# Kernel optimization log

Hardware: AMD Instinct MI355X
Metric: run time of the kernel (lower is better)

## Reference

```python
import jax, jax.numpy as jnp
import numpy as np


def setup_inputs() -> dict:
    key = jax.random.key(0)
    kq, kk, kv, km = jax.random.split(key, 4)
    B, H, S, D = 2, 16, 2048, 64
    Q = jax.random.normal(kq, (B, H, S, D), dtype=jnp.float32)
    K = jax.random.normal(kk, (B, H, S, D), dtype=jnp.float32)
    V = jax.random.normal(kv, (B, H, S, D), dtype=jnp.float32)
    mask = jax.random.randint(km, (B, 1, S, S), 0, 2).astype(jnp.bool_)
    return {"Q": Q, "K": K, "V": V, "mask": mask}


def reference(Q, K, V, mask):
    # scores: [B, H, Sq, Sk]
    scores = jnp.einsum("bhqd,bhkd->bhqk", Q, K)
    neg = jnp.finfo(scores.dtype).min
    # Faithful to original: mask fill happens BEFORE the sqrt(d) scaling.
    scores = jnp.where(mask, neg, scores)
    inv_sqrt_d = 1.0 / jnp.sqrt(jnp.asarray(Q.shape[-1], dtype=scores.dtype))
    attn = jax.nn.softmax(scores * inv_sqrt_d, axis=-1)
    return jnp.einsum("bhqk,bhkd->bhqd", attn, V)
```

## Files before the change

### kernel.cpp

```cpp
#include <hip/hip_runtime.h>
#include <stdint.h>


#define SQ 2048
#define DH 64

using bf16x8  = __attribute__((ext_vector_type(8)))  __bf16;
using f32x4   = __attribute__((ext_vector_type(4)))  float;
using ushort8 = __attribute__((ext_vector_type(8)))  unsigned short;
using ushort4v= __attribute__((ext_vector_type(4)))  unsigned short;
using u32x4   = __attribute__((ext_vector_type(4)))  unsigned int;

static __device__ __forceinline__ unsigned short f2bf(float f) {
    union { float f; uint32_t u; } c; c.f = f;
    return (unsigned short)((c.u + 0x8000u) >> 16);
}

static __device__ __forceinline__ uint32_t pkbf(float a, float b) {
    union { __bf16 h[2]; uint32_t u; } t;
    t.h[0] = (__bf16)a; t.h[1] = (__bf16)b;
    return t.u;
}

static __device__ __forceinline__ f32x4 mfma16(bf16x8 a, bf16x8 b, f32x4 c) {
    return __builtin_amdgcn_mfma_f32_16x16x32_bf16(a, b, c, 0, 0, 0);
}

static __device__ __forceinline__ void gload16(const void* g, void* l) {
    __builtin_amdgcn_global_load_lds(
        (const __attribute__((address_space(1))) void*)g,
        (__attribute__((address_space(3))) void*)l, 16, 0, 0);
}

__global__ __launch_bounds__(256)
void prep_kernel(const int* __restrict__ mask, const float* __restrict__ K,
                 const float* __restrict__ V, unsigned long long* __restrict__ words,
                 unsigned short* __restrict__ Kb, unsigned short* __restrict__ Vt) {
    __shared__ unsigned short tl[64][66];
    const int bx  = blockIdx.x;
    const int tid = threadIdx.x;
    if (bx < 32768) {
        int gid = bx * 256 + tid;
        int mv = mask[gid];
        unsigned long long b = __ballot(mv != 0);
        if ((gid & 63) == 0) words[gid >> 6] = b;
    } else if (bx < 36864) {
        int gid = (bx - 32768) * 256 + tid;
        float4 v = ((const float4*)K)[gid];
        ushort4v t;
        t[0]=f2bf(v.x); t[1]=f2bf(v.y); t[2]=f2bf(v.z); t[3]=f2bf(v.w);
        ((ushort4v*)Kb)[gid] = t;
    } else {
        const int vbx = bx - 36864;
        const int kt  = vbx & 31;
        const size_t bh = vbx >> 5;
        const float* vp = V + (bh * SQ + (size_t)kt * 64) * DH;
        #pragma unroll
        for (int i = 0; i < 4; ++i) {
            int idx = tid + 256 * i;
            int key = idx >> 4;
            int dc  = (idx & 15) * 4;
            float4 v = *(const float4*)(vp + (size_t)key * DH + dc);
            tl[key][dc + 0] = f2bf(v.x);
            tl[key][dc + 1] = f2bf(v.y);
            tl[key][dc + 2] = f2bf(v.z);
            tl[key][dc + 3] = f2bf(v.w);
        }
        __syncthreads();
        unsigned short* op = Vt + bh * DH * SQ + (size_t)kt * 64;
        #pragma unroll
        for (int i = 0; i < 4; ++i) {
            int idx = tid + 256 * i;
            int d  = idx >> 4;
            int m  = idx & 15;
            int kc = m * 4;
            int pos = 32 * (m >> 3) + 8 * (m & 3) + 4 * ((m >> 2) & 1);
            ushort4v t;
            t[0] = tl[kc + 0][d]; t[1] = tl[kc + 1][d];
            t[2] = tl[kc + 2][d]; t[3] = tl[kc + 3][d];
            *(ushort4v*)(op + (size_t)d * SQ + pos) = t;
        }
    }
}

__global__ __launch_bounds__(256, 4)
void attn_kernel(const float* __restrict__ Q,
                 const unsigned short* __restrict__ Kb,
                 const unsigned short* __restrict__ Vtg,
                 const unsigned long long* __restrict__ Mw,
                 float* __restrict__ out) {
    __shared__ __align__(16) unsigned short Ks[2][64 * 64];
    __shared__ __align__(16) unsigned short Vs[2][64 * 64];

    const int tid  = threadIdx.x;
    const int w    = tid >> 6;
    const int l    = tid & 63;
    const int quad = l >> 4;
    const int c16  = l & 15;
    const int bx = blockIdx.x;
    const int hh = bx & 15;
    const int b  = (bx >> 4) & 1;
    const int qt = bx >> 5;

    const size_t bh = (size_t)b * 16 + hh;
    const float* Qp = Q + bh * SQ * DH;
    const int qw = qt * 64 + 16 * w;

    const unsigned long long* Mrow = Mw + ((size_t)b * SQ + qw + c16) * (SQ / 64);

    const int s0 = (2 * w) * 64 + l;
    const int s1 = (2 * w + 1) * 64 + l;
    const int r0 = s0 >> 3, g0s = s0 & 7;
    const int r1 = s1 >> 3, g1s = s1 & 7;
    const char* Kg = (const char*)(Kb  + bh * (size_t)SQ * DH);
    const char* Vg = (const char*)(Vtg + bh * (size_t)DH * SQ);
    const char* kSrc0 = Kg + r0 * 128  + ((g0s ^ (r0 & 7)) << 4);
    const char* kSrc1 = Kg + r1 * 128  + ((g1s ^ (r1 & 7)) << 4);
    const char* vSrc0 = Vg + r0 * 4096 + ((g0s ^ (r0 & 7)) << 4);
    const char* vSrc1 = Vg + r1 * 4096 + ((g1s ^ (r1 & 7)) << 4);

    bf16x8 qf[2];
    {
        const float* qr = Qp + (size_t)(qw + c16) * DH;
        #pragma unroll
        for (int c = 0; c < 2; ++c) {
            int d0 = 32 * c + 8 * quad;
            float4 a  = *(const float4*)(qr + d0);
            float4 b4 = *(const float4*)(qr + d0 + 4);
            ushort8 t;
            t[0]=f2bf(a.x);  t[1]=f2bf(a.y);  t[2]=f2bf(a.z);  t[3]=f2bf(a.w);
            t[4]=f2bf(b4.x); t[5]=f2bf(b4.y); t[6]=f2bf(b4.z); t[7]=f2bf(b4.w);
            qf[c] = __builtin_bit_cast(bf16x8, t);
        }
    }

    f32x4 o[4];
    float lsum = 0.f;
    #pragma unroll
    for (int i = 0; i < 4; ++i) o[i] = (f32x4)(0.f);

    const int xg = (c16 & 7);
    int gfrag[2];
    #pragma unroll
    for (int c = 0; c < 2; ++c) gfrag[c] = ((4 * c + quad) ^ xg) << 3;

    unsigned long long mw = Mrow[0];
    gload16(kSrc0, &Ks[0][(2 * w) * 512]);
    gload16(kSrc1, &Ks[0][(2 * w + 1) * 512]);
    gload16(vSrc0, &Vs[0][(2 * w) * 512]);
    gload16(vSrc1, &Vs[0][(2 * w + 1) * 512]);
    kSrc0 += 8192; kSrc1 += 8192; vSrc0 += 128; vSrc1 += 128;
    __syncthreads();

    for (int t = 0; t < 32; ++t) {
        const int cur = t & 1;

        unsigned long long nmw = 0;
        if (t < 31) {
            gload16(kSrc0, &Ks[cur ^ 1][(2 * w) * 512]);
            gload16(kSrc1, &Ks[cur ^ 1][(2 * w + 1) * 512]);
            gload16(vSrc0, &Vs[cur ^ 1][(2 * w) * 512]);
            gload16(vSrc1, &Vs[cur ^ 1][(2 * w + 1) * 512]);
            kSrc0 += 8192; kSrc1 += 8192; vSrc0 += 128; vSrc1 += 128;
            nmw = Mrow[t + 1];
        }

        const unsigned short* Kc = Ks[cur];
        const unsigned short* Vc = Vs[cur];

        f32x4 s[4];
        #pragma unroll
        for (int i = 0; i < 4; ++i) s[i] = (f32x4)(0.f);
        __builtin_amdgcn_s_setprio(1);
        #pragma unroll
        for (int c = 0; c < 2; ++c) {
            #pragma unroll
            for (int nb = 0; nb < 4; ++nb) {
                bf16x8 kb = __builtin_bit_cast(bf16x8,
                    *(const ushort8*)&Kc[(c16 + 16 * nb) * 64 + gfrag[c]]);
                s[nb] = mfma16(kb, qf[c], s[nb]);
            }
        }
        __builtin_amdgcn_s_setprio(0);

        uint32_t pk[4][2];
        {
            const unsigned long long sh = mw >> (4 * quad);
            #pragma unroll
            for (int nb = 0; nb < 4; ++nb) {
                float pv[4];
                #pragma unroll
                for (int r = 0; r < 4; ++r) {
                    float e = __builtin_amdgcn_exp2f(fmaf(s[nb][r], 0.18033688f, -5.7707802f));
                    pv[r] = ((sh >> (16 * nb + r)) & 1ull) ? 0.0f : e;
                    lsum += pv[r];
                }
                pk[nb][0] = pkbf(pv[0], pv[1]);
                pk[nb][1] = pkbf(pv[2], pv[3]);
            }
        }

        bf16x8 pa[2];
        #pragma unroll
        for (int c = 0; c < 2; ++c) {
            u32x4 tv;
            tv[0] = pk[2 * c][0];     tv[1] = pk[2 * c][1];
            tv[2] = pk[2 * c + 1][0]; tv[3] = pk[2 * c + 1][1];
            pa[c] = __builtin_bit_cast(bf16x8, tv);
        }

        __builtin_amdgcn_s_setprio(1);
        #pragma unroll
        for (int c = 0; c < 2; ++c) {
            #pragma unroll
            for (int db = 0; db < 4; ++db) {
                bf16x8 vb = __builtin_bit_cast(bf16x8,
                    *(const ushort8*)&Vc[(c16 + 16 * db) * 64 + gfrag[c]]);
                o[db] = mfma16(vb, pa[c], o[db]);
            }
        }
        __builtin_amdgcn_s_setprio(0);

        __syncthreads();
        mw = nmw;
    }

    float v = lsum;
    v += __shfl_xor(v, 16, 64);
    v += __shfl_xor(v, 32, 64);
    const float rinv = 1.0f / v;
    float* op = out + (bh * SQ + (size_t)(qw + c16)) * DH + 4 * quad;
    #pragma unroll
    for (int db = 0; db < 4; ++db) {
        float4 st;
        st.x = o[db][0] * rinv; st.y = o[db][1] * rinv;
        st.z = o[db][2] * rinv; st.w = o[db][3] * rinv;
        *(float4*)(op + 16 * db) = st;
    }
}

extern "C" void kernel_launch(void* const* d_in, const int* in_sizes, int n_in,
                              void* d_out, int out_size, void* d_ws, size_t ws_size,
                              hipStream_t stream) {
    const float* Q    = (const float*)d_in[0];
    const float* K    = (const float*)d_in[1];
    const float* V    = (const float*)d_in[2];
    const int*   mask = (const int*)d_in[3];
    float* out = (float*)d_out;

    char* ws = (char*)d_ws;
    unsigned long long* mwords = (unsigned long long*)ws;
    unsigned short* Kb = (unsigned short*)(ws + (1 << 20));
    unsigned short* Vt = (unsigned short*)(ws + (1 << 20) + (8 << 20));

    prep_kernel<<<dim3(37888), dim3(256), 0, stream>>>(mask, K, V, mwords, Kb, Vt);
    attn_kernel<<<dim3(1024), dim3(256), 0, stream>>>(Q, Kb, Vt, mwords, out);
}
```

Baseline: 186.2 us.

## Switch attention kernel to 32x32x16 MFMA with split-K waves and LDS reduction

Replaces the 16x16x32 bf16 MFMA tiles with 32x32x16 tiles. Each pair of waves now covers 32 queries, and each wave of the pair handles half of the 64 keys in every tile. The V-transpose layout in the prep kernel is changed to match the new operand fragment order. Partial outputs and row sums from the two key-halves are combined through LDS at the end. The aim is fewer MFMA issues and fewer LDS fragment loads per tile, at the cost of a final cross-wave reduction and larger accumulator registers.

```diff
diff --git a/kernel.cpp b/kernel.cpp
--- a/kernel.cpp
+++ b/kernel.cpp
@@ -6,9 +6,10 @@
 #define DH 64
 
 using bf16x8  = __attribute__((ext_vector_type(8)))  __bf16;
-using f32x4   = __attribute__((ext_vector_type(4)))  float;
+using f32x16  = __attribute__((ext_vector_type(16))) float;
 using ushort8 = __attribute__((ext_vector_type(8)))  unsigned short;
 using ushort4v= __attribute__((ext_vector_type(4)))  unsigned short;
+using ushort2v= __attribute__((ext_vector_type(2)))  unsigned short;
 using u32x4   = __attribute__((ext_vector_type(4)))  unsigned int;
 
 static __device__ __forceinline__ unsigned short f2bf(float f) {
@@ -22,8 +23,8 @@
     return t.u;
 }
 
-static __device__ __forceinline__ f32x4 mfma16(bf16x8 a, bf16x8 b, f32x4 c) {
-    return __builtin_amdgcn_mfma_f32_16x16x32_bf16(a, b, c, 0, 0, 0);
+static __device__ __forceinline__ f32x16 mfma32(bf16x8 a, bf16x8 b, f32x16 c) {
+    return __builtin_amdgcn_mfma_f32_32x32x16_bf16(a, b, c, 0, 0, 0);
 }
 
 static __device__ __forceinline__ void gload16(const void* g, void* l) {
@@ -74,11 +75,12 @@
             int d  = idx >> 4;
             int m  = idx & 15;
             int kc = m * 4;
-            int pos = 32 * (m >> 3) + 8 * (m & 3) + 4 * ((m >> 2) & 1);
-            ushort4v t;
-            t[0] = tl[kc + 0][d]; t[1] = tl[kc + 1][d];
-            t[2] = tl[kc + 2][d]; t[3] = tl[kc + 3][d];
-            *(ushort4v*)(op + (size_t)d * SQ + pos) = t;
+            int base = 32 * ((m >> 3) & 1) + 8 * (m & 1) + 4 * ((m >> 2) & 1) + 2 * ((m >> 1) & 1);
+            ushort2v w0, w1;
+            w0[0] = tl[kc + 0][d]; w0[1] = tl[kc + 1][d];
+            w1[0] = tl[kc + 2][d]; w1[1] = tl[kc + 3][d];
+            *(ushort2v*)(op + (size_t)d * SQ + base)      = w0;
+            *(ushort2v*)(op + (size_t)d * SQ + base + 16) = w1;
         }
     }
 }
@@ -95,8 +97,10 @@
     const int tid  = threadIdx.x;
     const int w    = tid >> 6;
     const int l    = tid & 63;
-    const int quad = l >> 4;
-    const int c16  = l & 15;
+    const int qh   = w >> 1;
+    const int kh   = w & 1;
+    const int q5   = l & 31;
+    const int h    = l >> 5;
     const int bx = blockIdx.x;
     const int hh = bx & 15;
     const int b  = (bx >> 4) & 1;
@@ -104,9 +108,10 @@
 
     const size_t bh = (size_t)b * 16 + hh;
     const float* Qp = Q + bh * SQ * DH;
-    const int qw = qt * 64 + 16 * w;
-
-    const unsigned long long* Mrow = Mw + ((size_t)b * SQ + qw + c16) * (SQ / 64);
+    const int qbase = qt * 64 + 32 * qh;
+
+    const unsigned int* Mrow32 =
+        (const unsigned int*)(Mw + ((size_t)b * SQ + qbase + q5) * (SQ / 64)) + kh;
 
     const int s0 = (2 * w) * 64 + l;
     const int s1 = (2 * w + 1) * 64 + l;
@@ -119,12 +124,12 @@
     const char* vSrc0 = Vg + r0 * 4096 + ((g0s ^ (r0 & 7)) << 4);
     const char* vSrc1 = Vg + r1 * 4096 + ((g1s ^ (r1 & 7)) << 4);
 
-    bf16x8 qf[2];
+    bf16x8 qf[4];
     {
-        const float* qr = Qp + (size_t)(qw + c16) * DH;
-        #pragma unroll
-        for (int c = 0; c < 2; ++c) {
-            int d0 = 32 * c + 8 * quad;
+        const float* qr = Qp + (size_t)(qbase + q5) * DH;
+        #pragma unroll
+        for (int c = 0; c < 4; ++c) {
+            int d0 = 16 * c + 8 * h;
             float4 a  = *(const float4*)(qr + d0);
             float4 b4 = *(const float4*)(qr + d0 + 4);
             ushort8 t;
@@ -134,17 +139,25 @@
         }
     }
 
-    f32x4 o[4];
+    const int kr = 32 * kh + q5;
+    int kOff[4];
+    #pragma unroll
+    for (int c = 0; c < 4; ++c)
+        kOff[c] = kr * 128 + (((2 * c + h) ^ (kr & 7)) << 4);
+    int vOff[2][2];
+    #pragma unroll
+    for (int db = 0; db < 2; ++db) {
+        int d = 32 * db + q5;
+        #pragma unroll
+        for (int c = 0; c < 2; ++c)
+            vOff[db][c] = d * 128 + (((4 * kh + 2 * c + h) ^ (d & 7)) << 4);
+    }
+
+    f32x16 o[2];
     float lsum = 0.f;
-    #pragma unroll
-    for (int i = 0; i < 4; ++i) o[i] = (f32x4)(0.f);
-
-    const int xg = (c16 & 7);
-    int gfrag[2];
-    #pragma unroll
-    for (int c = 0; c < 2; ++c) gfrag[c] = ((4 * c + quad) ^ xg) << 3;
-
-    unsigned long long mw = Mrow[0];
+    o[0] = (f32x16)(0.f); o[1] = (f32x16)(0.f);
+
+    unsigned int mwh = Mrow32[0];
     gload16(kSrc0, &Ks[0][(2 * w) * 512]);
     gload16(kSrc1, &Ks[0][(2 * w + 1) * 512]);
     gload16(vSrc0, &Vs[0][(2 * w) * 512]);
@@ -155,87 +168,108 @@
     for (int t = 0; t < 32; ++t) {
         const int cur = t & 1;
 
-        unsigned long long nmw = 0;
+        unsigned int nmwh = 0;
         if (t < 31) {
             gload16(kSrc0, &Ks[cur ^ 1][(2 * w) * 512]);
             gload16(kSrc1, &Ks[cur ^ 1][(2 * w + 1) * 512]);
             gload16(vSrc0, &Vs[cur ^ 1][(2 * w) * 512]);
             gload16(vSrc1, &Vs[cur ^ 1][(2 * w + 1) * 512]);
             kSrc0 += 8192; kSrc1 += 8192; vSrc0 += 128; vSrc1 += 128;
-            nmw = Mrow[t + 1];
-        }
-
-        const unsigned short* Kc = Ks[cur];
-        const unsigned short* Vc = Vs[cur];
-
-        f32x4 s[4];
-        #pragma unroll
-        for (int i = 0; i < 4; ++i) s[i] = (f32x4)(0.f);
+            nmwh = Mrow32[2 * (t + 1)];
+        }
+
+        const char* Kc = (const char*)Ks + cur * 8192;
+        const char* Vc = (const char*)Vs + cur * 8192;
+
+        f32x16 s = (f32x16)(0.f);
         __builtin_amdgcn_s_setprio(1);
         #pragma unroll
-        for (int c = 0; c < 2; ++c) {
-            #pragma unroll
-            for (int nb = 0; nb < 4; ++nb) {
-                bf16x8 kb = __builtin_bit_cast(bf16x8,
-                    *(const ushort8*)&Kc[(c16 + 16 * nb) * 64 + gfrag[c]]);
-                s[nb] = mfma16(kb, qf[c], s[nb]);
-            }
+        for (int c = 0; c < 4; ++c) {
+            bf16x8 kb = __builtin_bit_cast(bf16x8, *(const ushort8*)(Kc + kOff[c]));
+            s = mfma32(kb, qf[c], s);
         }
         __builtin_amdgcn_s_setprio(0);
 
-        uint32_t pk[4][2];
-        {
-            const unsigned long long sh = mw >> (4 * quad);
-            #pragma unroll
-            for (int nb = 0; nb < 4; ++nb) {
-                float pv[4];
-                #pragma unroll
-                for (int r = 0; r < 4; ++r) {
-                    float e = __builtin_amdgcn_exp2f(fmaf(s[nb][r], 0.18033688f, -5.7707802f));
-                    pv[r] = ((sh >> (16 * nb + r)) & 1ull) ? 0.0f : e;
-                    lsum += pv[r];
-                }
-                pk[nb][0] = pkbf(pv[0], pv[1]);
-                pk[nb][1] = pkbf(pv[2], pv[3]);
-            }
-        }
-
+        const unsigned int mh = mwh >> (4 * h);
+        float pv[16];
+        float ts = 0.f;
+        #pragma unroll
+        for (int r = 0; r < 16; ++r) {
+            const int sh_amt = (r & 3) + 8 * (r >> 2);
+            float e = __builtin_amdgcn_exp2f(fmaf(s[r], 0.18033688f, -5.7707802f));
+            pv[r] = ((mh >> sh_amt) & 1u) ? 0.0f : e;
+            ts += pv[r];
+        }
+        lsum += ts;
+
+        unsigned int pk[4][2];
+        #pragma unroll
+        for (int g = 0; g < 4; ++g) {
+            pk[g][0] = pkbf(pv[4 * g + 0], pv[4 * g + 1]);
+            pk[g][1] = pkbf(pv[4 * g + 2], pv[4 * g + 3]);
+        }
         bf16x8 pa[2];
         #pragma unroll
         for (int c = 0; c < 2; ++c) {
             u32x4 tv;
-            tv[0] = pk[2 * c][0];     tv[1] = pk[2 * c][1];
-            tv[2] = pk[2 * c + 1][0]; tv[3] = pk[2 * c + 1][1];
+            tv[0] = pk[0][c]; tv[1] = pk[1][c]; tv[2] = pk[2][c]; tv[3] = pk[3][c];
             pa[c] = __builtin_bit_cast(bf16x8, tv);
         }
 
         __builtin_amdgcn_s_setprio(1);
         #pragma unroll
-        for (int c = 0; c < 2; ++c) {
+        for (int db = 0; db < 2; ++db) {
             #pragma unroll
-            for (int db = 0; db < 4; ++db) {
+            for (int c = 0; c < 2; ++c) {
                 bf16x8 vb = __builtin_bit_cast(bf16x8,
-                    *(const ushort8*)&Vc[(c16 + 16 * db) * 64 + gfrag[c]]);
-                o[db] = mfma16(vb, pa[c], o[db]);
+                    *(const ushort8*)(Vc + vOff[db][c]));
+                o[db] = mfma32(vb, pa[c], o[db]);
             }
         }
         __builtin_amdgcn_s_setprio(0);
 
         __syncthreads();
-        mw = nmw;
-    }
-
-    float v = lsum;
-    v += __shfl_xor(v, 16, 64);
-    v += __shfl_xor(v, 32, 64);
-    const float rinv = 1.0f / v;
-    float* op = out + (bh * SQ + (size_t)(qw + c16)) * DH + 4 * quad;
-    #pragma unroll
-    for (int db = 0; db < 4; ++db) {
-        float4 st;
-        st.x = o[db][0] * rinv; st.y = o[db][1] * rinv;
-        st.z = o[db][2] * rinv; st.w = o[db][3] * rinv;
-        *(float4*)(op + 16 * db) = st;
+        mwh = nmwh;
+    }
+
+    float lhalf = lsum;
+    lhalf += __shfl_xor(lhalf, 32, 64);
+    float* Ored = (float*)Ks;
+    float* Lred = (float*)Vs;
+    if (kh) {
+        #pragma unroll
+        for (int db = 0; db < 2; ++db) {
+            #pragma unroll
+            for (int g = 0; g < 4; ++g) {
+                int d0  = 32 * db + 8 * g + 4 * h;
+                int g16 = (d0 >> 2) ^ ((q5 & 7) << 1);
+                float4 st;
+                st.x = o[db][4 * g + 0]; st.y = o[db][4 * g + 1];
+                st.z = o[db][4 * g + 2]; st.w = o[db][4 * g + 3];
+                *(float4*)(Ored + qh * 2048 + q5 * 64 + g16 * 4) = st;
+            }
+        }
+        if (h == 0) Lred[qh * 32 + q5] = lhalf;
+    }
+    __syncthreads();
+    if (!kh) {
+        const float rinv = 1.0f / (lhalf + Lred[qh * 32 + q5]);
+        float* op = out + (bh * SQ + (size_t)(qbase + q5)) * DH;
+        #pragma unroll
+        for (int db = 0; db < 2; ++db) {
+            #pragma unroll
+            for (int g = 0; g < 4; ++g) {
+                int d0  = 32 * db + 8 * g + 4 * h;
+                int g16 = (d0 >> 2) ^ ((q5 & 7) << 1);
+                float4 pv4 = *(const float4*)(Ored + qh * 2048 + q5 * 64 + g16 * 4);
+                float4 st;
+                st.x = (o[db][4 * g + 0] + pv4.x) * rinv;
+                st.y = (o[db][4 * g + 1] + pv4.y) * rinv;
+                st.z = (o[db][4 * g + 2] + pv4.z) * rinv;
+                st.w = (o[db][4 * g + 3] + pv4.w) * rinv;
+                *(float4*)(op + d0) = st;
+            }
+        }
     }
 }
 
```

New measurement: 183.3 us. Within noise of the previous version (-1.5%).
